# Optimization experiments

Measured on AMD Instinct MI355X. Metric: run time of the kernel, lower is better.

## Reference

```python
import jax, jax.numpy as jnp
import numpy as np

B, N, D, H = 8, 1024, 1024, 16
HEAD_DIM = D // H
SCALING = HEAD_DIM ** (-0.5)
NEG = -1000000000.0


def setup_inputs() -> dict:
    key = jax.random.key(0)
    ks = jax.random.split(key, 7)
    x = jax.random.normal(ks[0], (B, N, D), dtype=jnp.float32)
    # variable-length batch: lengths in [N//2, N], mask[b, i] = i < len_b
    lengths = jax.random.randint(ks[1], (B,), N // 2, N + 1)
    mask = jnp.arange(N)[None, :] < lengths[:, None]  # [B, N] bool
    s = D ** (-0.5)
    Wk = jax.random.normal(ks[2], (D, D), dtype=jnp.float32) * s
    Wq = jax.random.normal(ks[3], (D, D), dtype=jnp.float32) * s
    Wv = jax.random.normal(ks[4], (D, D), dtype=jnp.float32) * s
    Wo = jax.random.normal(ks[5], (D, D), dtype=jnp.float32) * s
    bo = jnp.zeros((D,), dtype=jnp.float32)
    return {"x": x, "mask": mask, "Wk": Wk, "Wq": Wq, "Wv": Wv, "Wo": Wo, "bo": bo}


def reference(x, mask, Wk, Wq, Wv, Wo, bo):
    # torch nn.Linear: y = x @ W.T
    keys = (x @ Wk.T).reshape(B, N, H, HEAD_DIM)
    queries = (x @ Wq.T).reshape(B, N, H, HEAD_DIM)
    values = (x @ Wv.T).reshape(B, N, H, HEAD_DIM)
    # NOTE: faithful to source: keys on i, queries on j, softmax over j
    scores = jnp.einsum('bihx,bjhx->bhij', keys, queries) * SCALING  # [B,H,N,N]
    pair_mask = mask[:, None, :] & mask[:, :, None]                  # [B,N,N]
    scores = scores + jnp.where(pair_mask, 0.0, NEG)[:, None, :, :]
    attn = jax.nn.softmax(scores, axis=-1)
    out = jnp.einsum('bhij,bjhx->bihx', attn, values)                # [B,N,H,hd]
    out = out.reshape(B, N, D)
    out = out @ Wo.T + bo
    # source does out_dense[mask] (ragged); static-shape equivalent: zero padding
    return out * mask[:, :, None].astype(out.dtype)
```

## Files before the change

### kernel.cpp

```cpp
#include <hip/hip_runtime.h>

typedef unsigned short u16;
typedef __attribute__((ext_vector_type(8))) short short8;
typedef __attribute__((ext_vector_type(4))) short short4v;
typedef __attribute__((ext_vector_type(4))) float f32x4;
typedef __attribute__((ext_vector_type(16))) float f32x16;

#define MFMA16(a, b, c) __builtin_amdgcn_mfma_f32_16x16x32_bf16(a, b, c, 0, 0, 0)
#define MFMA32(a, b, c) __builtin_amdgcn_mfma_f32_32x32x16_bf16(a, b, c, 0, 0, 0)

#define BB 8
#define NN 1024
#define DD 1024
#define HH 16
#define HD 64
#define MM (BB * NN)
#define SCLOG2 0.18033688011112042f

static __device__ __forceinline__ u16 f2bf(float f) {
  unsigned u = __float_as_uint(f);
  u += 0x7fffu + ((u >> 16) & 1u);
  return (u16)(u >> 16);
}

static __device__ __forceinline__ void gld16(const void* g, void* l) {
  __builtin_amdgcn_global_load_lds((const __attribute__((address_space(1))) void*)g,
                                   (__attribute__((address_space(3))) void*)l, 16, 0, 0);
}

static __device__ __forceinline__ unsigned cvtpk(float lo, float hi) {
  unsigned r;
  asm("v_cvt_pk_bf16_f32 %0, %1, %2" : "=v"(r) : "v"(lo), "v"(hi));
  return r;
}

static __device__ __forceinline__ f32x16 zero16() {
  f32x16 v;
#pragma unroll
  for (int i = 0; i < 16; ++i) v[i] = 0.f;
  return v;
}

__global__ __launch_bounds__(256) void prep_kernel(const float* __restrict__ x,
                                                   const float* __restrict__ Wk, const float* __restrict__ Wq,
                                                   const float* __restrict__ Wv, const float* __restrict__ Wo,
                                                   u16* __restrict__ xb,
                                                   u16* __restrict__ wkb, u16* __restrict__ wqb,
                                                   u16* __restrict__ wvb, u16* __restrict__ wob,
                                                   const unsigned char* __restrict__ mask,
                                                   int* __restrict__ lens) {
  const int bid = blockIdx.x;
  const int t = threadIdx.x;
  if (bid == 6144) {
    __shared__ int acc[BB];
    if (t < BB) acc[t] = 0;
    __syncthreads();
    const bool isbyte = (mask[1] != 0);
    for (int bb = 0; bb < BB; ++bb) {
      int s = 0;
      if (isbyte) {
        for (int i = t; i < NN; i += 256) s += mask[(size_t)bb * NN + i] ? 1 : 0;
      } else {
        const int* mi = (const int*)mask;
        for (int i = t; i < NN; i += 256) s += mi[(size_t)bb * NN + i] != 0 ? 1 : 0;
      }
      if (s) atomicAdd(&acc[bb], s);
    }
    __syncthreads();
    if (t < BB) lens[t] = acc[t];
    return;
  }
  const float* in;
  u16* out;
  int i;
  if (bid < 4096) {
    in = x; out = xb; i = bid * 256 + t;
  } else {
    const int wi = bid - 4096;
    const int mat = wi >> 9;
    switch (mat) {
      case 0: in = Wk; out = wkb; break;
      case 1: in = Wq; out = wqb; break;
      case 2: in = Wv; out = wvb; break;
      default: in = Wo; out = wob; break;
    }
    i = (wi & 511) * 256 + t;
  }
  const f32x4* p = (const f32x4*)in + (size_t)i * 2;
  const f32x4 a = p[0], b = p[1];
  short8 o;
  o[0] = (short)f2bf(a[0]); o[1] = (short)f2bf(a[1]);
  o[2] = (short)f2bf(a[2]); o[3] = (short)f2bf(a[3]);
  o[4] = (short)f2bf(b[0]); o[5] = (short)f2bf(b[1]);
  o[6] = (short)f2bf(b[2]); o[7] = (short)f2bf(b[3]);
  *(short8*)(out + (size_t)i * 8) = o;
}

#define STAGE_G(d, k0_)                                                            \
  _Pragma("unroll") for (int p = 0; p < 2; ++p) {                                  \
    const int off = (p * 256 + t) * 16;                                            \
    const int row = off >> 6;                                                      \
    const int colb = (off & 63) ^ (((row >> 1) & 3) << 4);                         \
    gld16(Ag + (size_t)(m0 + row) * 1024 + (k0_) + (colb >> 1), &As[d][off >> 1]); \
    gld16(Bg + (size_t)(n0 + row) * 1024 + (k0_) + (colb >> 1), &Bs[d][off >> 1]); \
  }

#define GEMM_CORE2()                                                            \
  STAGE_G(0, 0)                                                                 \
  __syncthreads();                                                              \
  for (int k0 = 0; k0 < 1024; k0 += 32) {                                       \
    const int cur = (k0 >> 5) & 1;                                              \
    if (k0 + 32 < 1024) { STAGE_G(cur ^ 1, k0 + 32) }                           \
    short8 af[4], bf[4];                                                        \
    _Pragma("unroll") for (int mi = 0; mi < 4; ++mi) {                          \
      const int row = wr * 64 + mi * 16 + li;                                   \
      const int byo = row * 64 + ((lg * 16) ^ (((row >> 1) & 3) << 4));         \
      af[mi] = *(const short8*)((const char*)&As[cur][0] + byo);                \
    }                                                                           \
    _Pragma("unroll") for (int ni = 0; ni < 4; ++ni) {                          \
      const int row = wc * 64 + ni * 16 + li;                                   \
      const int byo = row * 64 + ((lg * 16) ^ (((row >> 1) & 3) << 4));         \
      bf[ni] = *(const short8*)((const char*)&Bs[cur][0] + byo);                \
    }                                                                           \
    __builtin_amdgcn_s_setprio(1);                                              \
    _Pragma("unroll") for (int mi = 0; mi < 4; ++mi)                            \
      _Pragma("unroll") for (int ni = 0; ni < 4; ++ni)                          \
          acc[mi][ni] = MFMA16(af[mi], bf[ni], acc[mi][ni]);                    \
    __builtin_amdgcn_s_setprio(0);                                              \
    __syncthreads();                                                            \
  }

__global__ __launch_bounds__(256) void gemm_qkv(const u16* __restrict__ A,
                                                const u16* __restrict__ Wk3, const u16* __restrict__ Wq3,
                                                const u16* __restrict__ Wv3,
                                                u16* __restrict__ kb, u16* __restrict__ qb,
                                                u16* __restrict__ vtb, const int* __restrict__ lens) {
  const int m0 = blockIdx.x * 128;
  if ((m0 & 1023) >= lens[m0 >> 10]) return;
  __shared__ u16 As[2][4096];
  __shared__ u16 Bs[2][4096];
  const int mat = blockIdx.y >> 3;
  const int n0 = (blockIdx.y & 7) * 128;
  const u16* Ag = A;
  const u16* Bg = (mat == 0) ? Wk3 : (mat == 1) ? Wq3 : Wv3;
  const int t = threadIdx.x;
  const int lane = t & 63;
  const int w = t >> 6;
  const int wr = w >> 1, wc = w & 1;
  const int li = lane & 15, lg = lane >> 4;
  f32x4 acc[4][4] = {};

  GEMM_CORE2()

  if (mat == 2) {
#pragma unroll
    for (int mi = 0; mi < 4; ++mi) {
      const int row = m0 + wr * 64 + mi * 16 + lg * 4;
      const int bb = row >> 10, jj = row & 1023;
#pragma unroll
      for (int ni = 0; ni < 4; ++ni) {
        const int col = n0 + wc * 64 + ni * 16 + li;
        const int h = col >> 6, x = col & 63;
        short4v st;
#pragma unroll
        for (int r = 0; r < 4; ++r) st[r] = (short)f2bf(acc[mi][ni][r]);
        *(short4v*)(vtb + ((size_t)((bb * HH + h) * HD + x)) * NN + jj) = st;
      }
    }
  } else {
    u16* C = (mat == 0) ? kb : qb;
    const float scale = (mat == 0) ? SCLOG2 : 1.0f;
#pragma unroll
    for (int mi = 0; mi < 4; ++mi)
#pragma unroll
      for (int ni = 0; ni < 4; ++ni) {
        const int col = n0 + wc * 64 + ni * 16 + li;
        const int rowb = m0 + wr * 64 + mi * 16 + lg * 4;
#pragma unroll
        for (int r = 0; r < 4; ++r)
          C[(size_t)(rowb + r) * 1024 + col] = f2bf(acc[mi][ni][r] * scale);
      }
  }
}

__global__ __launch_bounds__(256) void gemm_out(const u16* __restrict__ A, const u16* __restrict__ Bw,
                                                float* __restrict__ C, const float* __restrict__ bias,
                                                const int* __restrict__ lens) {
  const int m0 = blockIdx.x * 128;
  const int n0 = blockIdx.y * 128;
  const int t = threadIdx.x;
  if ((m0 & 1023) >= lens[m0 >> 10]) {
    const int r = t >> 1, ch = (t & 1) * 64;
    float* Crow = C + (size_t)(m0 + r) * 1024 + n0 + ch;
    const f32x4 z = {0.f, 0.f, 0.f, 0.f};
#pragma unroll
    for (int c = 0; c < 16; ++c) *(f32x4*)(Crow + c * 4) = z;
    return;
  }
  __shared__ u16 As[2][4096];
  __shared__ u16 Bs[2][4096];
  const u16* Ag = A;
  const u16* Bg = Bw;
  const int lane = t & 63;
  const int w = t >> 6;
  const int wr = w >> 1, wc = w & 1;
  const int li = lane & 15, lg = lane >> 4;
  f32x4 acc[4][4] = {};

  GEMM_CORE2()

#pragma unroll
  for (int ni = 0; ni < 4; ++ni) {
    const int col = n0 + wc * 64 + ni * 16 + li;
    const float bv = bias[col];
#pragma unroll
    for (int mi = 0; mi < 4; ++mi) {
      const int rowb = m0 + wr * 64 + mi * 16 + lg * 4;
#pragma unroll
      for (int r = 0; r < 4; ++r) {
        const int row = rowb + r;
        const int bb = row >> 10, ii = row & 1023;
        const float v = (ii < lens[bb]) ? (acc[mi][ni][r] + bv) : 0.f;
        C[(size_t)row * 1024 + col] = v;
      }
    }
  }
}

#define QK_PART(JC, SN0_, SN1_)                                                \
  { const u16* Qc = &Qs[(JC) & 1][0];                                          \
    SN0_ = zero16(); SN1_ = zero16();                                          \
    __builtin_amdgcn_s_setprio(1);                                             \
    _Pragma("unroll") for (int ks = 0; ks < 4; ++ks) {                         \
      const short8 qf = *(const short8*)(Qc + (ks * 64 + l) * 8);              \
      SN0_ = MFMA32(qf, kf[ks], SN0_); }                                       \
    _Pragma("unroll") for (int ks = 0; ks < 4; ++ks) {                         \
      const short8 qf = *(const short8*)(Qc + ((4 + ks) * 64 + l) * 8);        \
      SN1_ = MFMA32(qf, kf[ks], SN1_); }                                       \
    __builtin_amdgcn_s_setprio(0); }

#define V_READ(JC, VF_)                                                        \
  { const u16* Vc = &Vs[(JC) & 1][0];                                          \
    _Pragma("unroll") for (int kk = 0; kk < 8; ++kk)                           \
      VF_[kk] = *(const short8*)(Vc + (kk * 64 + l) * 8); }

#define SM_PV(S0_, S1_, VF_)                                                   \
  {                                                                            \
    float tmx[8];                                                              \
    _Pragma("unroll") for (int r = 0; r < 8; ++r)                              \
      tmx[r] = fmaxf(fmaxf(S0_[r], S0_[r + 8]), fmaxf(S1_[r], S1_[r + 8]));    \
    _Pragma("unroll") for (int r = 0; r < 4; ++r)                              \
      tmx[r] = fmaxf(tmx[r], tmx[r + 4]);                                      \
    float pmax = fmaxf(fmaxf(tmx[0], tmx[1]), fmaxf(tmx[2], tmx[3]));          \
    pmax = fmaxf(pmax, __shfl_xor(pmax, 32));                                  \
    if (!__all(pmax <= m_run + 11.5f)) {                    \
      const float mnew = fmaxf(m_run, pmax);                                   \
      const float al = __builtin_amdgcn_exp2f(m_run - mnew);                   \
      l_run *= al;                                                             \
      _Pragma("unroll") for (int r = 0; r < 16; ++r) { o0[r] *= al; o1[r] *= al; } \
      m_run = mnew;                                                            \
    }                                                                          \
    float ac0 = 0.f, ac1 = 0.f, ac2 = 0.f, ac3 = 0.f;                          \
    _Pragma("unroll") for (int r = 0; r < 16; r += 4) {                        \
      const float p0 = __builtin_amdgcn_exp2f(S0_[r + 0] - m_run);             \
      const float p1 = __builtin_amdgcn_exp2f(S0_[r + 1] - m_run);             \
      const float p2 = __builtin_amdgcn_exp2f(S0_[r + 2] - m_run);             \
      const float p3 = __builtin_amdgcn_exp2f(S0_[r + 3] - m_run);             \
      S0_[r + 0] = p0; S0_[r + 1] = p1; S0_[r + 2] = p2; S0_[r + 3] = p3;      \
      ac0 += p0; ac1 += p1; ac2 += p2; ac3 += p3;                              \
    }                                                                          \
    _Pragma("unroll") for (int r = 0; r < 16; r += 4) {                        \
      const float p0 = __builtin_amdgcn_exp2f(S1_[r + 0] - m_run);             \
      const float p1 = __builtin_amdgcn_exp2f(S1_[r + 1] - m_run);             \
      const float p2 = __builtin_amdgcn_exp2f(S1_[r + 2] - m_run);             \
      const float p3 = __builtin_amdgcn_exp2f(S1_[r + 3] - m_run);             \
      S1_[r + 0] = p0; S1_[r + 1] = p1; S1_[r + 2] = p2; S1_[r + 3] = p3;      \
      ac0 += p0; ac1 += p1; ac2 += p2; ac3 += p3;                              \
    }                                                                          \
    float rs = (ac0 + ac1) + (ac2 + ac3);                                      \
    rs += __shfl_xor(rs, 32);                                                  \
    l_run += rs;                                                               \
    short8 pf[4];                                                              \
    _Pragma("unroll") for (int jk = 0; jk < 4; ++jk) {                         \
      const f32x16& ss = (jk < 2) ? S0_ : S1_;                                 \
      const int kk2 = jk & 1;                                                  \
      unsigned W0 = cvtpk(ss[8 * kk2 + 0], ss[8 * kk2 + 1]);                   \
      unsigned W1 = cvtpk(ss[8 * kk2 + 2], ss[8 * kk2 + 3]);                   \
      unsigned W2 = cvtpk(ss[8 * kk2 + 4], ss[8 * kk2 + 5]);                   \
      unsigned W3 = cvtpk(ss[8 * kk2 + 6], ss[8 * kk2 + 7]);                   \
      asm("v_permlane32_swap_b32 %0, %1" : "+v"(W0), "+v"(W2));                \
      asm("v_permlane32_swap_b32 %0, %1" : "+v"(W1), "+v"(W3));                \
      union { unsigned u[4]; short8 s; } pu;                                   \
      pu.u[0] = W0; pu.u[1] = W1; pu.u[2] = W2; pu.u[3] = W3;                  \
      pf[jk] = pu.s;                                                           \
    }                                                                          \
    __builtin_amdgcn_s_setprio(1);                                             \
    _Pragma("unroll") for (int kg = 0; kg < 4; ++kg) o0 = MFMA32(VF_[kg], pf[kg], o0); \
    _Pragma("unroll") for (int kg = 0; kg < 4; ++kg) o1 = MFMA32(VF_[4 + kg], pf[kg], o1); \
    __builtin_amdgcn_s_setprio(0);                                             \
  }

#define MASK_LAST(S0_, S1_)                                                    \
  { const int j0m = (nt - 1) * 64;                                             \
    if (j0m + 64 > len) {                                                      \
      _Pragma("unroll") for (int r = 0; r < 16; ++r) {                         \
        const int jl = (r & 3) + 8 * (r >> 2) + 4 * hi;                        \
        if (j0m + jl >= len) S0_[r] = -3.0e38f;                                \
        if (j0m + 32 + jl >= len) S1_[r] = -3.0e38f;                           \
      } } }

#define ATTN_BODY(JT, SP0, SP1, VFP, SN0, SN1, VFN)                            \
  { const int jc = (JT);                                                       \
    if (jc + 1 < nt) STAGE((jc + 1) & 1, (jc + 1) * 64);                       \
    QK_PART(jc, SN0, SN1)                                                      \
    SM_PV(SP0, SP1, VFP)                                                       \
    V_READ(jc, VFN)                                                            \
    __syncthreads(); }

__global__ __launch_bounds__(256) void attn_kernel(const u16* __restrict__ Kb, const u16* __restrict__ Qb,
                                                   const u16* __restrict__ Vtb, u16* __restrict__ attb,
                                                   const int* __restrict__ lens) {
  const int bid = blockIdx.x;
  const int b = bid >> 7;
  const int ic = (bid >> 3) & 7;
  const int h = ((bid & 7) << 1) | ((bid >> 6) & 1);
  const int len = lens[b];
  const int i0 = ic * 128;
  if (i0 >= len) return;
  const int t = threadIdx.x;
  const int w = t >> 6, l = t & 63;
  const int l31 = l & 31, hi = l >> 5;
  const int i0w = i0 + w * 32;

  __shared__ u16 Qs[2][4096];
  __shared__ u16 Vs[2][4096];

  short8 kf[4];
  {
    const u16* kp = Kb + ((size_t)(b * NN + i0w + l31)) * DD + h * HD + hi * 8;
#pragma unroll
    for (int ks = 0; ks < 4; ++ks) kf[ks] = *(const short8*)(kp + ks * 16);
  }

  const size_t qsrc = ((size_t)(b * NN) + l31) * DD + h * HD + w * 16 + hi * 8;
  const size_t vsrc = ((size_t)((b * HH + h) * HD + l31)) * NN + w * 16 + hi * 8;

  auto STAGE = [&](int buf, int j0) {
    u16* qd = &Qs[buf][0] + t * 8;
    u16* vd = &Vs[buf][0] + t * 8;
    gld16(Qb + qsrc + (size_t)j0 * DD, qd);
    gld16(Qb + qsrc + (size_t)(j0 + 32) * DD, qd + 2048);
    gld16(Vtb + vsrc + j0, vd);
    gld16(Vtb + vsrc + 32 * NN + j0, vd + 2048);
  };

  f32x16 o0 = zero16(), o1 = zero16();
  float m_run = -3.0e38f, l_run = 0.f;
  const int nt = (len + 63) >> 6;

  f32x16 sA0, sA1, sB0, sB1;
  short8 vfA[8], vfB[8];

  STAGE(0, 0);
  __syncthreads();
  if (nt > 1) STAGE(1, 64);
  QK_PART(0, sA0, sA1)
  V_READ(0, vfA)
  __syncthreads();

  int jt = 1;
  for (; jt + 1 < nt; jt += 2) {
    ATTN_BODY(jt, sA0, sA1, vfA, sB0, sB1, vfB)
    ATTN_BODY(jt + 1, sB0, sB1, vfB, sA0, sA1, vfA)
  }
  if (jt < nt) {
    ATTN_BODY(jt, sA0, sA1, vfA, sB0, sB1, vfB)
    MASK_LAST(sB0, sB1)
    SM_PV(sB0, sB1, vfB)
  } else {
    MASK_LAST(sA0, sA1)
    SM_PV(sA0, sA1, vfA)
  }

  const float inv = 1.f / l_run;
  u16* op = attb + (size_t)(b * NN + i0w + l31) * DD + h * HD + hi * 4;
#pragma unroll
  for (int xs = 0; xs < 2; ++xs) {
    const f32x16& oo = xs ? o1 : o0;
#pragma unroll
    for (int q = 0; q < 4; ++q) {
      short4v st;
#pragma unroll
      for (int e = 0; e < 4; ++e) st[e] = (short)f2bf(oo[q * 4 + e] * inv);
      *(short4v*)(op + xs * 32 + q * 8) = st;
    }
  }
}

extern "C" void kernel_launch(void* const* d_in, const int* in_sizes, int n_in,
                              void* d_out, int out_size, void* d_ws, size_t ws_size,
                              hipStream_t stream) {
  const float* x = (const float*)d_in[0];
  const unsigned char* mask = (const unsigned char*)d_in[1];
  const float* Wk = (const float*)d_in[2];
  const float* Wq = (const float*)d_in[3];
  const float* Wv = (const float*)d_in[4];
  const float* Wo = (const float*)d_in[5];
  const float* bo = (const float*)d_in[6];
  float* out = (float*)d_out;

  char* ws = (char*)d_ws;
  size_t o = 0;
  int* lens = (int*)(ws + o); o += 256;
  u16* xb  = (u16*)(ws + o); o += (size_t)MM * DD * 2;
  u16* wkb = (u16*)(ws + o); o += (size_t)DD * DD * 2;
  u16* wqb = (u16*)(ws + o); o += (size_t)DD * DD * 2;
  u16* wvb = (u16*)(ws + o); o += (size_t)DD * DD * 2;
  u16* wob = (u16*)(ws + o); o += (size_t)DD * DD * 2;
  u16* kb  = (u16*)(ws + o); o += (size_t)MM * DD * 2;
  u16* qb  = (u16*)(ws + o); o += (size_t)MM * DD * 2;
  u16* vtb = (u16*)(ws + o); o += (size_t)MM * DD * 2;
  u16* attb = xb;

  prep_kernel<<<dim3(6145), dim3(256), 0, stream>>>(x, Wk, Wq, Wv, Wo, xb, wkb, wqb, wvb,
                                                    wob, mask, lens);

  gemm_qkv<<<dim3(MM / 128, 24), dim3(256), 0, stream>>>(xb, wkb, wqb, wvb, kb, qb, vtb, lens);

  attn_kernel<<<dim3(1024), dim3(256), 0, stream>>>(kb, qb, vtb, attb, lens);

  gemm_out<<<dim3(MM / 128, DD / 128), dim3(256), 0, stream>>>(attb, wob, out, bo, lens);
}
```

Before: 178.0 us.

## Compute two B tiles per block in QKV and output GEMMs to reuse A

Each GEMM block now loads one A tile and two B tiles per k-step and keeps two accumulator sets. For QKV, K and Q for the same columns share a block, and V blocks cover 256 columns. The output GEMM covers 256 columns per block. This halves the A-tile global loads and the block count, at the cost of double the accumulator registers and more LDS per block, which may reduce occupancy.

```diff
diff --git a/kernel.cpp b/kernel.cpp
--- a/kernel.cpp
+++ b/kernel.cpp
@@ -96,22 +96,24 @@
   *(short8*)(out + (size_t)i * 8) = o;
 }
 
-#define STAGE_G(d, k0_)                                                            \
-  _Pragma("unroll") for (int p = 0; p < 2; ++p) {                                  \
-    const int off = (p * 256 + t) * 16;                                            \
-    const int row = off >> 6;                                                      \
-    const int colb = (off & 63) ^ (((row >> 1) & 3) << 4);                         \
-    gld16(Ag + (size_t)(m0 + row) * 1024 + (k0_) + (colb >> 1), &As[d][off >> 1]); \
-    gld16(Bg + (size_t)(n0 + row) * 1024 + (k0_) + (colb >> 1), &Bs[d][off >> 1]); \
-  }
-
-#define GEMM_CORE2()                                                            \
-  STAGE_G(0, 0)                                                                 \
+#define STAGE_D(d, k0_)                                                             \
+  _Pragma("unroll") for (int p = 0; p < 2; ++p) {                                   \
+    const int off = (p * 256 + t) * 16;                                             \
+    const int row = off >> 6;                                                       \
+    const int colb = (off & 63) ^ (((row >> 1) & 3) << 4);                          \
+    const int gofs = (k0_) + (colb >> 1);                                           \
+    gld16(Ag + (size_t)(m0 + row) * 1024 + gofs, &As[d][off >> 1]);                 \
+    gld16(B1g + (size_t)(n1 + row) * 1024 + gofs, &B1s[d][off >> 1]);               \
+    gld16(B2g + (size_t)(n2 + row) * 1024 + gofs, &B2s[d][off >> 1]);               \
+  }
+
+#define GEMM_CORE_D()                                                           \
+  STAGE_D(0, 0)                                                                 \
   __syncthreads();                                                              \
   for (int k0 = 0; k0 < 1024; k0 += 32) {                                       \
     const int cur = (k0 >> 5) & 1;                                              \
-    if (k0 + 32 < 1024) { STAGE_G(cur ^ 1, k0 + 32) }                           \
-    short8 af[4], bf[4];                                                        \
+    if (k0 + 32 < 1024) { STAGE_D(cur ^ 1, k0 + 32) }                           \
+    short8 af[4], b1f[4], b2f[4];                                               \
     _Pragma("unroll") for (int mi = 0; mi < 4; ++mi) {                          \
       const int row = wr * 64 + mi * 16 + li;                                   \
       const int byo = row * 64 + ((lg * 16) ^ (((row >> 1) & 3) << 4));         \
@@ -120,12 +122,15 @@
     _Pragma("unroll") for (int ni = 0; ni < 4; ++ni) {                          \
       const int row = wc * 64 + ni * 16 + li;                                   \
       const int byo = row * 64 + ((lg * 16) ^ (((row >> 1) & 3) << 4));         \
-      bf[ni] = *(const short8*)((const char*)&Bs[cur][0] + byo);                \
+      b1f[ni] = *(const short8*)((const char*)&B1s[cur][0] + byo);              \
+      b2f[ni] = *(const short8*)((const char*)&B2s[cur][0] + byo);              \
     }                                                                           \
     __builtin_amdgcn_s_setprio(1);                                              \
     _Pragma("unroll") for (int mi = 0; mi < 4; ++mi)                            \
-      _Pragma("unroll") for (int ni = 0; ni < 4; ++ni)                          \
-          acc[mi][ni] = MFMA16(af[mi], bf[ni], acc[mi][ni]);                    \
+      _Pragma("unroll") for (int ni = 0; ni < 4; ++ni) {                        \
+        acc1[mi][ni] = MFMA16(af[mi], b1f[ni], acc1[mi][ni]);                   \
+        acc2[mi][ni] = MFMA16(af[mi], b2f[ni], acc2[mi][ni]);                   \
+      }                                                                         \
     __builtin_amdgcn_s_setprio(0);                                              \
     __syncthreads();                                                            \
   }
@@ -138,48 +143,57 @@
   const int m0 = blockIdx.x * 128;
   if ((m0 & 1023) >= lens[m0 >> 10]) return;
   __shared__ u16 As[2][4096];
-  __shared__ u16 Bs[2][4096];
-  const int mat = blockIdx.y >> 3;
-  const int n0 = (blockIdx.y & 7) * 128;
+  __shared__ u16 B1s[2][4096];
+  __shared__ u16 B2s[2][4096];
+  const int y = blockIdx.y;
+  const bool kq = (y < 8);
   const u16* Ag = A;
-  const u16* Bg = (mat == 0) ? Wk3 : (mat == 1) ? Wq3 : Wv3;
+  const u16* B1g = kq ? Wk3 : Wv3;
+  const u16* B2g = kq ? Wq3 : Wv3;
+  const int n1 = kq ? y * 128 : (y - 8) * 256;
+  const int n2 = kq ? n1 : n1 + 128;
   const int t = threadIdx.x;
   const int lane = t & 63;
   const int w = t >> 6;
   const int wr = w >> 1, wc = w & 1;
   const int li = lane & 15, lg = lane >> 4;
-  f32x4 acc[4][4] = {};
-
-  GEMM_CORE2()
-
-  if (mat == 2) {
+  f32x4 acc1[4][4] = {};
+  f32x4 acc2[4][4] = {};
+
+  GEMM_CORE_D()
+
+  if (kq) {
+#pragma unroll
+    for (int mi = 0; mi < 4; ++mi)
+#pragma unroll
+      for (int ni = 0; ni < 4; ++ni) {
+        const int col = n1 + wc * 64 + ni * 16 + li;
+        const int rowb = m0 + wr * 64 + mi * 16 + lg * 4;
+#pragma unroll
+        for (int r = 0; r < 4; ++r) {
+          kb[(size_t)(rowb + r) * 1024 + col] = f2bf(acc1[mi][ni][r] * SCLOG2);
+          qb[(size_t)(rowb + r) * 1024 + col] = f2bf(acc2[mi][ni][r]);
+        }
+      }
+  } else {
 #pragma unroll
     for (int mi = 0; mi < 4; ++mi) {
       const int row = m0 + wr * 64 + mi * 16 + lg * 4;
       const int bb = row >> 10, jj = row & 1023;
 #pragma unroll
       for (int ni = 0; ni < 4; ++ni) {
-        const int col = n0 + wc * 64 + ni * 16 + li;
-        const int h = col >> 6, x = col & 63;
-        short4v st;
-#pragma unroll
-        for (int r = 0; r < 4; ++r) st[r] = (short)f2bf(acc[mi][ni][r]);
-        *(short4v*)(vtb + ((size_t)((bb * HH + h) * HD + x)) * NN + jj) = st;
+        const int c1 = n1 + wc * 64 + ni * 16 + li;
+        const int c2 = n2 + wc * 64 + ni * 16 + li;
+        short4v s1, s2;
+#pragma unroll
+        for (int r = 0; r < 4; ++r) {
+          s1[r] = (short)f2bf(acc1[mi][ni][r]);
+          s2[r] = (short)f2bf(acc2[mi][ni][r]);
+        }
+        *(short4v*)(vtb + ((size_t)((bb * HH + (c1 >> 6)) * HD + (c1 & 63))) * NN + jj) = s1;
+        *(short4v*)(vtb + ((size_t)((bb * HH + (c2 >> 6)) * HD + (c2 & 63))) * NN + jj) = s2;
       }
     }
-  } else {
-    u16* C = (mat == 0) ? kb : qb;
-    const float scale = (mat == 0) ? SCLOG2 : 1.0f;
-#pragma unroll
-    for (int mi = 0; mi < 4; ++mi)
-#pragma unroll
-      for (int ni = 0; ni < 4; ++ni) {
-        const int col = n0 + wc * 64 + ni * 16 + li;
-        const int rowb = m0 + wr * 64 + mi * 16 + lg * 4;
-#pragma unroll
-        for (int r = 0; r < 4; ++r)
-          C[(size_t)(rowb + r) * 1024 + col] = f2bf(acc[mi][ni][r] * scale);
-      }
   }
 }
 
@@ -187,32 +201,38 @@
                                                 float* __restrict__ C, const float* __restrict__ bias,
                                                 const int* __restrict__ lens) {
   const int m0 = blockIdx.x * 128;
-  const int n0 = blockIdx.y * 128;
+  const int n1 = blockIdx.y * 256;
+  const int n2 = n1 + 128;
   const int t = threadIdx.x;
   if ((m0 & 1023) >= lens[m0 >> 10]) {
-    const int r = t >> 1, ch = (t & 1) * 64;
-    float* Crow = C + (size_t)(m0 + r) * 1024 + n0 + ch;
+    const int r = t >> 1, ch = (t & 1) * 128;
+    float* Crow = C + (size_t)(m0 + r) * 1024 + n1 + ch;
     const f32x4 z = {0.f, 0.f, 0.f, 0.f};
 #pragma unroll
-    for (int c = 0; c < 16; ++c) *(f32x4*)(Crow + c * 4) = z;
+    for (int c = 0; c < 32; ++c) *(f32x4*)(Crow + c * 4) = z;
     return;
   }
   __shared__ u16 As[2][4096];
-  __shared__ u16 Bs[2][4096];
+  __shared__ u16 B1s[2][4096];
+  __shared__ u16 B2s[2][4096];
   const u16* Ag = A;
-  const u16* Bg = Bw;
+  const u16* B1g = Bw;
+  const u16* B2g = Bw;
   const int lane = t & 63;
   const int w = t >> 6;
   const int wr = w >> 1, wc = w & 1;
   const int li = lane & 15, lg = lane >> 4;
-  f32x4 acc[4][4] = {};
-
-  GEMM_CORE2()
+  f32x4 acc1[4][4] = {};
+  f32x4 acc2[4][4] = {};
+
+  GEMM_CORE_D()
 
 #pragma unroll
   for (int ni = 0; ni < 4; ++ni) {
-    const int col = n0 + wc * 64 + ni * 16 + li;
-    const float bv = bias[col];
+    const int c1 = n1 + wc * 64 + ni * 16 + li;
+    const int c2 = n2 + wc * 64 + ni * 16 + li;
+    const float bv1 = bias[c1];
+    const float bv2 = bias[c2];
 #pragma unroll
     for (int mi = 0; mi < 4; ++mi) {
       const int rowb = m0 + wr * 64 + mi * 16 + lg * 4;
@@ -220,8 +240,9 @@
       for (int r = 0; r < 4; ++r) {
         const int row = rowb + r;
         const int bb = row >> 10, ii = row & 1023;
-        const float v = (ii < lens[bb]) ? (acc[mi][ni][r] + bv) : 0.f;
-        C[(size_t)row * 1024 + col] = v;
+        const bool live = ii < lens[bb];
+        C[(size_t)row * 1024 + c1] = live ? (acc1[mi][ni][r] + bv1) : 0.f;
+        C[(size_t)row * 1024 + c2] = live ? (acc2[mi][ni][r] + bv2) : 0.f;
       }
     }
   }
@@ -425,9 +446,9 @@
   prep_kernel<<<dim3(6145), dim3(256), 0, stream>>>(x, Wk, Wq, Wv, Wo, xb, wkb, wqb, wvb,
                                                     wob, mask, lens);
 
-  gemm_qkv<<<dim3(MM / 128, 24), dim3(256), 0, stream>>>(xb, wkb, wqb, wvb, kb, qb, vtb, lens);
+  gemm_qkv<<<dim3(MM / 128, 12), dim3(256), 0, stream>>>(xb, wkb, wqb, wvb, kb, qb, vtb, lens);
 
   attn_kernel<<<dim3(1024), dim3(256), 0, stream>>>(kb, qb, vtb, attb, lens);
 
-  gemm_out<<<dim3(MM / 128, DD / 128), dim3(256), 0, stream>>>(attb, wob, out, bo, lens);
-}
+  gemm_out<<<dim3(MM / 128, 4), dim3(256), 0, stream>>>(attb, wob, out, bo, lens);
+}
```

Measured after the change: 224.2 us. 26.0% more time.
